# Kernel optimization log

Measured on AMD Instinct MI355X. Metric: run time of the kernel, lower is better.

The kernel has to match this reference:

```python
import jax, jax.numpy as jnp
import numpy as np

N, INSIZE, K, D = 512, 512, 64, 16


def setup_inputs() -> dict:
    key = jax.random.key(0)
    k1, k2, k3 = jax.random.split(key, 3)
    x = jax.random.normal(k1, (N, INSIZE), dtype=jnp.float32)
    W = jax.random.normal(k2, (K * D, INSIZE), dtype=jnp.float32) * (1.0 / np.sqrt(INSIZE))
    b = jax.random.normal(k3, (K * D,), dtype=jnp.float32) * 0.01
    return {"x": x, "W": W, "b": b}


def reference(x, W, b):
    # Linear: [N, insize] -> [N, K*D] -> [N, K, D]
    feat = (x @ W.T + b).reshape(-1, K, D)
    n = feat.shape[0]
    # Pairwise L1 distance over D: norm[i, k, j] = sum_d |feat[i,k,d] - feat[j,k,d]|
    # feature [N,K,D,1] vs feature_ [1,K,D,N] in the original broadcast
    diff = jnp.abs(feat[:, :, :, None] - jnp.transpose(feat, (1, 2, 0))[None])  # [N,K,D,N]
    norm = jnp.sum(diff, axis=2)  # [N,K,N]
    # Eraser: suppress self-similarity on the diagonal with a large penalty
    eraser = jnp.eye(n, dtype=feat.dtype)[:, None, :]  # [N,1,N]
    c_b = jnp.exp(-(norm + eraser * 1e6))
    o_b = jnp.sum(c_b, axis=2)  # [N,K]
    return jnp.concatenate((x, o_b), axis=1)  # [N, insize+K]
```

## Files before the change

kernel.cpp:

```cpp
#include <hip/hip_runtime.h>

#define NPTS 512
#define INS  512
#define KDIM 64
#define DDIM 16
#define CDIM (KDIM*DDIM)
#define OUTC (INS + KDIM)

__device__ __forceinline__ float exp2_fast(float x) {
    return __builtin_amdgcn_exp2f(x);
}

__global__ __launch_bounds__(256) void gemm_kernel(
    const float* __restrict__ x,
    const float* __restrict__ W,
    const float* __restrict__ bias,
    float* __restrict__ featT)
{
    const int tid = threadIdx.x;
    const int cbase = blockIdx.x * 64;
    const int ibase = blockIdx.y * 32;

    __shared__ float xs[16][32 + 2];
    __shared__ float wss[16][64 + 4];

    const int tx = tid & 15;
    const int ty = tid >> 4;

    float acc[2][4] = {};

    const int kkL = tid & 15;
    const int rL  = tid >> 4;

    for (int k0 = 0; k0 < INS; k0 += 16) {
        xs[kkL][rL]      = x[(ibase + rL) * INS + k0 + kkL];
        xs[kkL][rL + 16] = x[(ibase + rL + 16) * INS + k0 + kkL];
        wss[kkL][rL]      = W[(cbase + rL) * INS + k0 + kkL];
        wss[kkL][rL + 16] = W[(cbase + rL + 16) * INS + k0 + kkL];
        wss[kkL][rL + 32] = W[(cbase + rL + 32) * INS + k0 + kkL];
        wss[kkL][rL + 48] = W[(cbase + rL + 48) * INS + k0 + kkL];
        __syncthreads();

        #pragma unroll
        for (int kk = 0; kk < 16; ++kk) {
            float2 a = *(const float2*)&xs[kk][ty * 2];
            float4 w = *(const float4*)&wss[kk][tx * 4];
            acc[0][0] += a.x * w.x;  acc[0][1] += a.x * w.y;
            acc[0][2] += a.x * w.z;  acc[0][3] += a.x * w.w;
            acc[1][0] += a.y * w.x;  acc[1][1] += a.y * w.y;
            acc[1][2] += a.y * w.z;  acc[1][3] += a.y * w.w;
        }
        __syncthreads();
    }

    const float LOG2E = 1.4426950408889634f;
    const int c = cbase + tx * 4;
    float4 bq = *(const float4*)&bias[c];
    const int k = c >> 4;
    const int d = c & 15;
    #pragma unroll
    for (int ii = 0; ii < 2; ++ii) {
        const int i = ibase + ty * 2 + ii;
        float4 v;
        v.x = (acc[ii][0] + bq.x) * LOG2E;
        v.y = (acc[ii][1] + bq.y) * LOG2E;
        v.z = (acc[ii][2] + bq.z) * LOG2E;
        v.w = (acc[ii][3] + bq.w) * LOG2E;
        *(float4*)&featT[(k * NPTS + i) * DDIM + d] = v;
    }
}

__global__ __launch_bounds__(256) void pairwise_kernel(
    const float* __restrict__ featT,
    float* __restrict__ out)
{
    const int k = blockIdx.x;
    const int ibase = blockIdx.y * 64;

    __shared__ float fj[NPTS * DDIM];
    __shared__ float part[4][64];

    {
        const float4* src = (const float4*)(featT + (size_t)k * NPTS * DDIM);
        float4* dst = (float4*)fj;
        #pragma unroll
        for (int t = 0; t < 8; ++t)
            dst[threadIdx.x + t * 256] = src[threadIdx.x + t * 256];
    }

    const int lane = threadIdx.x & 63;
    const int wv   = threadIdx.x >> 6;
    const int i    = ibase + lane;

    float fi[16];
    {
        const float4* p = (const float4*)(featT + ((size_t)k * NPTS + i) * DDIM);
        float4 v0 = p[0], v1 = p[1], v2 = p[2], v3 = p[3];
        fi[0]=v0.x; fi[1]=v0.y; fi[2]=v0.z; fi[3]=v0.w;
        fi[4]=v1.x; fi[5]=v1.y; fi[6]=v1.z; fi[7]=v1.w;
        fi[8]=v2.x; fi[9]=v2.y; fi[10]=v2.z; fi[11]=v2.w;
        fi[12]=v3.x; fi[13]=v3.y; fi[14]=v3.z; fi[15]=v3.w;
    }
    __syncthreads();

    float acc0 = 0.f, acc1 = 0.f;
    const float* fp = fj + wv * 128 * DDIM;
    #pragma unroll 1
    for (int jj = 0; jj < 128; jj += 2) {
        {
            float n0=0.f, n1=0.f, n2=0.f, n3=0.f;
            #pragma unroll
            for (int d = 0; d < 4; ++d) {
                n0 += fabsf(fi[d]      - fp[d]);
                n1 += fabsf(fi[d + 4]  - fp[d + 4]);
                n2 += fabsf(fi[d + 8]  - fp[d + 8]);
                n3 += fabsf(fi[d + 12] - fp[d + 12]);
            }
            acc0 += exp2_fast(-((n0 + n1) + (n2 + n3)));
        }
        {
            float n0=0.f, n1=0.f, n2=0.f, n3=0.f;
            #pragma unroll
            for (int d = 0; d < 4; ++d) {
                n0 += fabsf(fi[d]      - fp[DDIM + d]);
                n1 += fabsf(fi[d + 4]  - fp[DDIM + d + 4]);
                n2 += fabsf(fi[d + 8]  - fp[DDIM + d + 8]);
                n3 += fabsf(fi[d + 12] - fp[DDIM + d + 12]);
            }
            acc1 += exp2_fast(-((n0 + n1) + (n2 + n3)));
        }
        fp += 2 * DDIM;
    }

    part[wv][lane] = acc0 + acc1;
    __syncthreads();

    if (wv == 0) {
        float o = ((part[0][lane] + part[1][lane]) + (part[2][lane] + part[3][lane])) - 1.0f;
        out[(size_t)i * OUTC + INS + k] = o;
    }
}

__global__ __launch_bounds__(256) void copy_x_kernel(
    const float* __restrict__ x, float* __restrict__ out)
{
    const int idx = blockIdx.x * 256 + threadIdx.x;
    const int i  = idx >> 7;
    const int j4 = idx & 127;
    ((float4*)out)[i * (OUTC / 4) + j4] = ((const float4*)x)[idx];
}

extern "C" void kernel_launch(void* const* d_in, const int* in_sizes, int n_in,
                              void* d_out, int out_size, void* d_ws, size_t ws_size,
                              hipStream_t stream) {
    const float* x    = (const float*)d_in[0];
    const float* W    = (const float*)d_in[1];
    const float* bias = (const float*)d_in[2];
    float* out = (float*)d_out;
    float* featT = (float*)d_ws;

    gemm_kernel<<<dim3(CDIM / 64, NPTS / 32), 256, 0, stream>>>(x, W, bias, featT);
    copy_x_kernel<<<dim3(NPTS * (INS / 4) / 256), 256, 0, stream>>>(x, out);
    pairwise_kernel<<<dim3(KDIM, NPTS / 64), 256, 0, stream>>>(featT, out);
}
```

Baseline: 106.2 us.

## Split-K GEMM into partial buffers and tile pairwise over j with atomics

The GEMM is split four ways along the input dimension. Each split writes a partial feature buffer, and the pairwise kernel sums the four partials when it loads them. The pairwise kernel is retiled so each block covers 128 i-rows against a 128-point j-quarter, with each thread handling two i rows per shared j load, and results are accumulated with atomicAdd into an output pre-initialized to -1. This raises the number of blocks and the register reuse of shared loads, at the cost of four times the workspace traffic, repeated partial summation in every block, and float atomics with nondeterministic ordering.

```diff
diff --git a/kernel.cpp b/kernel.cpp
--- a/kernel.cpp
+++ b/kernel.cpp
@@ -6,6 +6,8 @@
 #define DDIM 16
 #define CDIM (KDIM*DDIM)
 #define OUTC (INS + KDIM)
+#define KSPLIT 4
+#define FEAT_ELEMS ((size_t)NPTS * CDIM)
 
 __device__ __forceinline__ float exp2_fast(float x) {
     return __builtin_amdgcn_exp2f(x);
@@ -20,6 +22,7 @@
     const int tid = threadIdx.x;
     const int cbase = blockIdx.x * 64;
     const int ibase = blockIdx.y * 32;
+    const int kbase = blockIdx.z * (INS / KSPLIT);
 
     __shared__ float xs[16][32 + 2];
     __shared__ float wss[16][64 + 4];
@@ -32,7 +35,7 @@
     const int kkL = tid & 15;
     const int rL  = tid >> 4;
 
-    for (int k0 = 0; k0 < INS; k0 += 16) {
+    for (int k0 = kbase; k0 < kbase + INS / KSPLIT; k0 += 16) {
         xs[kkL][rL]      = x[(ibase + rL) * INS + k0 + kkL];
         xs[kkL][rL + 16] = x[(ibase + rL + 16) * INS + k0 + kkL];
         wss[kkL][rL]      = W[(cbase + rL) * INS + k0 + kkL];
@@ -54,100 +57,141 @@
     }
 
     const float LOG2E = 1.4426950408889634f;
+    const float bsel = (blockIdx.z == 0) ? 1.0f : 0.0f;
     const int c = cbase + tx * 4;
     float4 bq = *(const float4*)&bias[c];
     const int k = c >> 4;
     const int d = c & 15;
+    float* dst = featT + (size_t)blockIdx.z * FEAT_ELEMS;
     #pragma unroll
     for (int ii = 0; ii < 2; ++ii) {
         const int i = ibase + ty * 2 + ii;
         float4 v;
-        v.x = (acc[ii][0] + bq.x) * LOG2E;
-        v.y = (acc[ii][1] + bq.y) * LOG2E;
-        v.z = (acc[ii][2] + bq.z) * LOG2E;
-        v.w = (acc[ii][3] + bq.w) * LOG2E;
-        *(float4*)&featT[(k * NPTS + i) * DDIM + d] = v;
-    }
-}
-
-__global__ __launch_bounds__(256) void pairwise_kernel(
-    const float* __restrict__ featT,
+        v.x = (acc[ii][0] + bq.x * bsel) * LOG2E;
+        v.y = (acc[ii][1] + bq.y * bsel) * LOG2E;
+        v.z = (acc[ii][2] + bq.z * bsel) * LOG2E;
+        v.w = (acc[ii][3] + bq.w * bsel) * LOG2E;
+        *(float4*)&dst[((size_t)k * NPTS + i) * DDIM + d] = v;
+    }
+}
+
+__global__ __launch_bounds__(256) void init_out_kernel(
+    const float* __restrict__ x, float* __restrict__ out)
+{
+    const int idx = blockIdx.x * 256 + threadIdx.x;
+    const int i  = idx / (OUTC / 4);
+    const int j4 = idx - i * (OUTC / 4);
+    float4 v;
+    if (j4 < INS / 4) {
+        v = ((const float4*)x)[i * (INS / 4) + j4];
+    } else {
+        v = make_float4(-1.0f, -1.0f, -1.0f, -1.0f);
+    }
+    ((float4*)out)[idx] = v;
+}
+
+__device__ __forceinline__ void load_feat16(
+    const float* f0, const float* f1, const float* f2, const float* f3,
+    size_t off, float* fi)
+{
+    #pragma unroll
+    for (int q = 0; q < 4; ++q) {
+        float4 a = *(const float4*)(f0 + off + q * 4);
+        float4 b = *(const float4*)(f1 + off + q * 4);
+        float4 c = *(const float4*)(f2 + off + q * 4);
+        float4 d = *(const float4*)(f3 + off + q * 4);
+        fi[q * 4 + 0] = (a.x + b.x) + (c.x + d.x);
+        fi[q * 4 + 1] = (a.y + b.y) + (c.y + d.y);
+        fi[q * 4 + 2] = (a.z + b.z) + (c.z + d.z);
+        fi[q * 4 + 3] = (a.w + b.w) + (c.w + d.w);
+    }
+}
+
+__global__ __launch_bounds__(256, 4) void pairwise_kernel(
+    const float* __restrict__ f0, const float* __restrict__ f1,
+    const float* __restrict__ f2, const float* __restrict__ f3,
     float* __restrict__ out)
 {
-    const int k = blockIdx.x;
-    const int ibase = blockIdx.y * 64;
-
-    __shared__ float fj[NPTS * DDIM];
-    __shared__ float part[4][64];
+    const int k     = blockIdx.x;
+    const int itile = blockIdx.y;
+    const int jq    = blockIdx.z;
+
+    __shared__ float fj[128 * DDIM];
+    __shared__ float part[4][128];
 
     {
-        const float4* src = (const float4*)(featT + (size_t)k * NPTS * DDIM);
+        const size_t base = ((size_t)k * NPTS + jq * 128) * DDIM;
+        const float4* s0 = (const float4*)(f0 + base);
+        const float4* s1 = (const float4*)(f1 + base);
+        const float4* s2 = (const float4*)(f2 + base);
+        const float4* s3 = (const float4*)(f3 + base);
         float4* dst = (float4*)fj;
         #pragma unroll
-        for (int t = 0; t < 8; ++t)
-            dst[threadIdx.x + t * 256] = src[threadIdx.x + t * 256];
+        for (int u = 0; u < 2; ++u) {
+            int idx = threadIdx.x + u * 256;
+            float4 a = s0[idx], b = s1[idx], c = s2[idx], d = s3[idx];
+            float4 r;
+            r.x = (a.x + b.x) + (c.x + d.x);
+            r.y = (a.y + b.y) + (c.y + d.y);
+            r.z = (a.z + b.z) + (c.z + d.z);
+            r.w = (a.w + b.w) + (c.w + d.w);
+            dst[idx] = r;
+        }
     }
 
     const int lane = threadIdx.x & 63;
     const int wv   = threadIdx.x >> 6;
-    const int i    = ibase + lane;
-
-    float fi[16];
-    {
-        const float4* p = (const float4*)(featT + ((size_t)k * NPTS + i) * DDIM);
-        float4 v0 = p[0], v1 = p[1], v2 = p[2], v3 = p[3];
-        fi[0]=v0.x; fi[1]=v0.y; fi[2]=v0.z; fi[3]=v0.w;
-        fi[4]=v1.x; fi[5]=v1.y; fi[6]=v1.z; fi[7]=v1.w;
-        fi[8]=v2.x; fi[9]=v2.y; fi[10]=v2.z; fi[11]=v2.w;
-        fi[12]=v3.x; fi[13]=v3.y; fi[14]=v3.z; fi[15]=v3.w;
-    }
+    const int i0   = itile * 128 + lane;
+    const int i1   = i0 + 64;
+
+    float fi0[16], fi1[16];
+    load_feat16(f0, f1, f2, f3, ((size_t)k * NPTS + i0) * DDIM, fi0);
+    load_feat16(f0, f1, f2, f3, ((size_t)k * NPTS + i1) * DDIM, fi1);
     __syncthreads();
 
     float acc0 = 0.f, acc1 = 0.f;
-    const float* fp = fj + wv * 128 * DDIM;
-    #pragma unroll 1
-    for (int jj = 0; jj < 128; jj += 2) {
+    const float* fp = fj + wv * 32 * DDIM;
+    #pragma unroll 2
+    for (int jj = 0; jj < 32; ++jj) {
+        const float* p = fp + jj * DDIM;
+        float4 q0 = *(const float4*)(p);
+        float4 q1 = *(const float4*)(p + 4);
+        float4 q2 = *(const float4*)(p + 8);
+        float4 q3 = *(const float4*)(p + 12);
         {
-            float n0=0.f, n1=0.f, n2=0.f, n3=0.f;
-            #pragma unroll
-            for (int d = 0; d < 4; ++d) {
-                n0 += fabsf(fi[d]      - fp[d]);
-                n1 += fabsf(fi[d + 4]  - fp[d + 4]);
-                n2 += fabsf(fi[d + 8]  - fp[d + 8]);
-                n3 += fabsf(fi[d + 12] - fp[d + 12]);
-            }
-            acc0 += exp2_fast(-((n0 + n1) + (n2 + n3)));
+            float a0 = fabsf(fi0[0]  - q0.x) + fabsf(fi0[1]  - q0.y)
+                     + fabsf(fi0[2]  - q0.z) + fabsf(fi0[3]  - q0.w);
+            float a1 = fabsf(fi0[4]  - q1.x) + fabsf(fi0[5]  - q1.y)
+                     + fabsf(fi0[6]  - q1.z) + fabsf(fi0[7]  - q1.w);
+            float a2 = fabsf(fi0[8]  - q2.x) + fabsf(fi0[9]  - q2.y)
+                     + fabsf(fi0[10] - q2.z) + fabsf(fi0[11] - q2.w);
+            float a3 = fabsf(fi0[12] - q3.x) + fabsf(fi0[13] - q3.y)
+                     + fabsf(fi0[14] - q3.z) + fabsf(fi0[15] - q3.w);
+            acc0 += exp2_fast(-((a0 + a1) + (a2 + a3)));
         }
         {
-            float n0=0.f, n1=0.f, n2=0.f, n3=0.f;
-            #pragma unroll
-            for (int d = 0; d < 4; ++d) {
-                n0 += fabsf(fi[d]      - fp[DDIM + d]);
-                n1 += fabsf(fi[d + 4]  - fp[DDIM + d + 4]);
-                n2 += fabsf(fi[d + 8]  - fp[DDIM + d + 8]);
-                n3 += fabsf(fi[d + 12] - fp[DDIM + d + 12]);
-            }
-            acc1 += exp2_fast(-((n0 + n1) + (n2 + n3)));
-        }
-        fp += 2 * DDIM;
-    }
-
-    part[wv][lane] = acc0 + acc1;
+            float b0 = fabsf(fi1[0]  - q0.x) + fabsf(fi1[1]  - q0.y)
+                     + fabsf(fi1[2]  - q0.z) + fabsf(fi1[3]  - q0.w);
+            float b1 = fabsf(fi1[4]  - q1.x) + fabsf(fi1[5]  - q1.y)
+                     + fabsf(fi1[6]  - q1.z) + fabsf(fi1[7]  - q1.w);
+            float b2 = fabsf(fi1[8]  - q2.x) + fabsf(fi1[9]  - q2.y)
+                     + fabsf(fi1[10] - q2.z) + fabsf(fi1[11] - q2.w);
+            float b3 = fabsf(fi1[12] - q3.x) + fabsf(fi1[13] - q3.y)
+                     + fabsf(fi1[14] - q3.z) + fabsf(fi1[15] - q3.w);
+            acc1 += exp2_fast(-((b0 + b1) + (b2 + b3)));
+        }
+    }
+
+    part[wv][lane]      = acc0;
+    part[wv][lane + 64] = acc1;
     __syncthreads();
 
-    if (wv == 0) {
-        float o = ((part[0][lane] + part[1][lane]) + (part[2][lane] + part[3][lane])) - 1.0f;
-        out[(size_t)i * OUTC + INS + k] = o;
-    }
-}
-
-__global__ __launch_bounds__(256) void copy_x_kernel(
-    const float* __restrict__ x, float* __restrict__ out)
-{
-    const int idx = blockIdx.x * 256 + threadIdx.x;
-    const int i  = idx >> 7;
-    const int j4 = idx & 127;
-    ((float4*)out)[i * (OUTC / 4) + j4] = ((const float4*)x)[idx];
+    if (threadIdx.x < 128) {
+        float s = (part[0][threadIdx.x] + part[1][threadIdx.x])
+                + (part[2][threadIdx.x] + part[3][threadIdx.x]);
+        const int i = itile * 128 + threadIdx.x;
+        atomicAdd(&out[(size_t)i * OUTC + INS + k], s);
+    }
 }
 
 extern "C" void kernel_launch(void* const* d_in, const int* in_sizes, int n_in,
@@ -159,7 +203,8 @@
     float* out = (float*)d_out;
     float* featT = (float*)d_ws;
 
-    gemm_kernel<<<dim3(CDIM / 64, NPTS / 32), 256, 0, stream>>>(x, W, bias, featT);
-    copy_x_kernel<<<dim3(NPTS * (INS / 4) / 256), 256, 0, stream>>>(x, out);
-    pairwise_kernel<<<dim3(KDIM, NPTS / 64), 256, 0, stream>>>(featT, out);
-}
+    gemm_kernel<<<dim3(CDIM / 64, NPTS / 32, KSPLIT), 256, 0, stream>>>(x, W, bias, featT);
+    init_out_kernel<<<dim3(NPTS * (OUTC / 4) / 256), 256, 0, stream>>>(x, out);
+    pairwise_kernel<<<dim3(KDIM, 4, 4), 256, 0, stream>>>(
+        featT, featT + FEAT_ELEMS, featT + 2 * FEAT_ELEMS, featT + 3 * FEAT_ELEMS, out);
+}
```

Result: faster. 97.68 us (-8.0%).

## Split-K GEMM, fused reduce/init kernel, and j-split pairwise with atomics

Applied to the files above, without the earlier changes.

The GEMM becomes split-K with 8 partial outputs and larger 64x64 tiles. A new kernel reduces the partials, adds bias and the log2e scale, copies x into the output, and initialises the o_b columns to -1. The pairwise kernel now splits j into 8 chunks, and each thread handles 4 i rows to reuse j loads from shared memory. Partial sums are accumulated into the output with atomicAdd. This raises parallelism and cuts shared-memory footprint, at the cost of extra workspace traffic, atomics, and nondeterministic summation order.

```diff
diff --git a/kernel.cpp b/kernel.cpp
--- a/kernel.cpp
+++ b/kernel.cpp
@@ -6,148 +6,174 @@
 #define DDIM 16
 #define CDIM (KDIM*DDIM)
 #define OUTC (INS + KDIM)
+#define KSPLIT 8
+#define FEAT_ELEMS ((size_t)NPTS * CDIM)
+#define FEAT_F4    (FEAT_ELEMS / 4)
 
 __device__ __forceinline__ float exp2_fast(float x) {
     return __builtin_amdgcn_exp2f(x);
 }
 
+__device__ __forceinline__ void fma2(float2& acc, float s, float x, float y) {
+    acc.x = __builtin_fmaf(s, x, acc.x);
+    acc.y = __builtin_fmaf(s, y, acc.y);
+}
+
 __global__ __launch_bounds__(256) void gemm_kernel(
     const float* __restrict__ x,
     const float* __restrict__ W,
-    const float* __restrict__ bias,
     float* __restrict__ featT)
 {
     const int tid = threadIdx.x;
     const int cbase = blockIdx.x * 64;
-    const int ibase = blockIdx.y * 32;
+    const int ibase = blockIdx.y * 64;
+    const int kbase = blockIdx.z * (INS / KSPLIT);
 
-    __shared__ float xs[16][32 + 2];
-    __shared__ float wss[16][64 + 4];
+    __shared__ float xs[16][68];
+    __shared__ float wss[16][68];
 
     const int tx = tid & 15;
     const int ty = tid >> 4;
-
-    float acc[2][4] = {};
-
     const int kkL = tid & 15;
     const int rL  = tid >> 4;
 
-    for (int k0 = 0; k0 < INS; k0 += 16) {
-        xs[kkL][rL]      = x[(ibase + rL) * INS + k0 + kkL];
-        xs[kkL][rL + 16] = x[(ibase + rL + 16) * INS + k0 + kkL];
-        wss[kkL][rL]      = W[(cbase + rL) * INS + k0 + kkL];
-        wss[kkL][rL + 16] = W[(cbase + rL + 16) * INS + k0 + kkL];
-        wss[kkL][rL + 32] = W[(cbase + rL + 32) * INS + k0 + kkL];
-        wss[kkL][rL + 48] = W[(cbase + rL + 48) * INS + k0 + kkL];
+    float2 acc[4][2] = {};
+
+    for (int k0 = kbase; k0 < kbase + INS / KSPLIT; k0 += 16) {
+        #pragma unroll
+        for (int q = 0; q < 4; ++q) {
+            xs[kkL][rL + 16 * q]  = x[(ibase + rL + 16 * q) * INS + k0 + kkL];
+            wss[kkL][rL + 16 * q] = W[(cbase + rL + 16 * q) * INS + k0 + kkL];
+        }
         __syncthreads();
 
         #pragma unroll
         for (int kk = 0; kk < 16; ++kk) {
-            float2 a = *(const float2*)&xs[kk][ty * 2];
+            float4 a = *(const float4*)&xs[kk][ty * 4];
             float4 w = *(const float4*)&wss[kk][tx * 4];
-            acc[0][0] += a.x * w.x;  acc[0][1] += a.x * w.y;
-            acc[0][2] += a.x * w.z;  acc[0][3] += a.x * w.w;
-            acc[1][0] += a.y * w.x;  acc[1][1] += a.y * w.y;
-            acc[1][2] += a.y * w.z;  acc[1][3] += a.y * w.w;
+            fma2(acc[0][0], a.x, w.x, w.y);  fma2(acc[0][1], a.x, w.z, w.w);
+            fma2(acc[1][0], a.y, w.x, w.y);  fma2(acc[1][1], a.y, w.z, w.w);
+            fma2(acc[2][0], a.z, w.x, w.y);  fma2(acc[2][1], a.z, w.z, w.w);
+            fma2(acc[3][0], a.w, w.x, w.y);  fma2(acc[3][1], a.w, w.z, w.w);
         }
         __syncthreads();
     }
 
-    const float LOG2E = 1.4426950408889634f;
     const int c = cbase + tx * 4;
-    float4 bq = *(const float4*)&bias[c];
     const int k = c >> 4;
     const int d = c & 15;
+    float* dst = featT + (size_t)blockIdx.z * FEAT_ELEMS;
     #pragma unroll
-    for (int ii = 0; ii < 2; ++ii) {
-        const int i = ibase + ty * 2 + ii;
-        float4 v;
-        v.x = (acc[ii][0] + bq.x) * LOG2E;
-        v.y = (acc[ii][1] + bq.y) * LOG2E;
-        v.z = (acc[ii][2] + bq.z) * LOG2E;
-        v.w = (acc[ii][3] + bq.w) * LOG2E;
-        *(float4*)&featT[(k * NPTS + i) * DDIM + d] = v;
+    for (int ii = 0; ii < 4; ++ii) {
+        const int i = ibase + ty * 4 + ii;
+        float4 v = make_float4(acc[ii][0].x, acc[ii][0].y, acc[ii][1].x, acc[ii][1].y);
+        *(float4*)&dst[((size_t)k * NPTS + i) * DDIM + d] = v;
     }
 }
 
-__global__ __launch_bounds__(256) void pairwise_kernel(
+__global__ __launch_bounds__(256) void fuse_reduce_init_kernel(
     const float* __restrict__ featT,
+    const float* __restrict__ bias,
+    const float* __restrict__ x,
+    float* __restrict__ featR,
     float* __restrict__ out)
 {
-    const int k = blockIdx.x;
-    const int ibase = blockIdx.y * 64;
+    const int b = blockIdx.x;
+    if (b < 512) {
+        const int f4 = b * 256 + threadIdx.x;
+        const float4* s = (const float4*)featT;
+        float4 p0 = s[f4];
+        float4 p1 = s[f4 + 1 * FEAT_F4];
+        float4 p2 = s[f4 + 2 * FEAT_F4];
+        float4 p3 = s[f4 + 3 * FEAT_F4];
+        float4 p4 = s[f4 + 4 * FEAT_F4];
+        float4 p5 = s[f4 + 5 * FEAT_F4];
+        float4 p6 = s[f4 + 6 * FEAT_F4];
+        float4 p7 = s[f4 + 7 * FEAT_F4];
+        const int k = f4 >> 11;
+        const float4 bq = ((const float4*)bias)[(k << 2) + (f4 & 3)];
+        const float LOG2E = 1.4426950408889634f;
+        float4 r;
+        r.x = (((p0.x + p1.x) + (p2.x + p3.x)) + ((p4.x + p5.x) + (p6.x + p7.x)) + bq.x) * LOG2E;
+        r.y = (((p0.y + p1.y) + (p2.y + p3.y)) + ((p4.y + p5.y) + (p6.y + p7.y)) + bq.y) * LOG2E;
+        r.z = (((p0.z + p1.z) + (p2.z + p3.z)) + ((p4.z + p5.z) + (p6.z + p7.z)) + bq.z) * LOG2E;
+        r.w = (((p0.w + p1.w) + (p2.w + p3.w)) + ((p4.w + p5.w) + (p6.w + p7.w)) + bq.w) * LOG2E;
+        ((float4*)featR)[f4] = r;
+    } else {
+        const int idx = (b - 512) * 256 + threadIdx.x;
+        const int i  = idx / (OUTC / 4);
+        const int j4 = idx - i * (OUTC / 4);
+        float4 v;
+        if (j4 < INS / 4) v = ((const float4*)x)[i * (INS / 4) + j4];
+        else              v = make_float4(-1.0f, -1.0f, -1.0f, -1.0f);
+        ((float4*)out)[idx] = v;
+    }
+}
 
-    __shared__ float fj[NPTS * DDIM];
-    __shared__ float part[4][64];
+__global__ __launch_bounds__(256, 4) void pairwise_kernel(
+    const float* __restrict__ featR,
+    float* __restrict__ out)
+{
+    const int k     = blockIdx.x;
+    const int itile = blockIdx.y;
+    const int jq    = blockIdx.z;
 
-    {
-        const float4* src = (const float4*)(featT + (size_t)k * NPTS * DDIM);
-        float4* dst = (float4*)fj;
-        #pragma unroll
-        for (int t = 0; t < 8; ++t)
-            dst[threadIdx.x + t * 256] = src[threadIdx.x + t * 256];
-    }
+    __shared__ float fj[64 * DDIM];
+    __shared__ float part[4][256];
+
+    ((float4*)fj)[threadIdx.x] =
+        ((const float4*)(featR + ((size_t)k * NPTS + jq * 64) * DDIM))[threadIdx.x];
 
     const int lane = threadIdx.x & 63;
     const int wv   = threadIdx.x >> 6;
-    const int i    = ibase + lane;
 
-    float fi[16];
-    {
-        const float4* p = (const float4*)(featT + ((size_t)k * NPTS + i) * DDIM);
+    float fi[4][16];
+    #pragma unroll
+    for (int u = 0; u < 4; ++u) {
+        const int i = itile * 256 + u * 64 + lane;
+        const float4* p = (const float4*)(featR + ((size_t)k * NPTS + i) * DDIM);
         float4 v0 = p[0], v1 = p[1], v2 = p[2], v3 = p[3];
-        fi[0]=v0.x; fi[1]=v0.y; fi[2]=v0.z; fi[3]=v0.w;
-        fi[4]=v1.x; fi[5]=v1.y; fi[6]=v1.z; fi[7]=v1.w;
-        fi[8]=v2.x; fi[9]=v2.y; fi[10]=v2.z; fi[11]=v2.w;
-        fi[12]=v3.x; fi[13]=v3.y; fi[14]=v3.z; fi[15]=v3.w;
+        fi[u][0]=v0.x;  fi[u][1]=v0.y;  fi[u][2]=v0.z;  fi[u][3]=v0.w;
+        fi[u][4]=v1.x;  fi[u][5]=v1.y;  fi[u][6]=v1.z;  fi[u][7]=v1.w;
+        fi[u][8]=v2.x;  fi[u][9]=v2.y;  fi[u][10]=v2.z; fi[u][11]=v2.w;
+        fi[u][12]=v3.x; fi[u][13]=v3.y; fi[u][14]=v3.z; fi[u][15]=v3.w;
     }
     __syncthreads();
 
-    float acc0 = 0.f, acc1 = 0.f;
-    const float* fp = fj + wv * 128 * DDIM;
-    #pragma unroll 1
-    for (int jj = 0; jj < 128; jj += 2) {
-        {
-            float n0=0.f, n1=0.f, n2=0.f, n3=0.f;
-            #pragma unroll
-            for (int d = 0; d < 4; ++d) {
-                n0 += fabsf(fi[d]      - fp[d]);
-                n1 += fabsf(fi[d + 4]  - fp[d + 4]);
-                n2 += fabsf(fi[d + 8]  - fp[d + 8]);
-                n3 += fabsf(fi[d + 12] - fp[d + 12]);
-            }
-            acc0 += exp2_fast(-((n0 + n1) + (n2 + n3)));
+    float acc[4] = {0.f, 0.f, 0.f, 0.f};
+    const float* fp = fj + wv * 16 * DDIM;
+    #pragma unroll 2
+    for (int jj = 0; jj < 16; ++jj) {
+        const float* p = fp + jj * DDIM;
+        float4 q0 = *(const float4*)(p);
+        float4 q1 = *(const float4*)(p + 4);
+        float4 q2 = *(const float4*)(p + 8);
+        float4 q3 = *(const float4*)(p + 12);
+        #pragma unroll
+        for (int u = 0; u < 4; ++u) {
+            float a0 = fabsf(fi[u][0]  - q0.x) + fabsf(fi[u][1]  - q0.y)
+                     + fabsf(fi[u][2]  - q0.z) + fabsf(fi[u][3]  - q0.w);
+            float a1 = fabsf(fi[u][4]  - q1.x) + fabsf(fi[u][5]  - q1.y)
+                     + fabsf(fi[u][6]  - q1.z) + fabsf(fi[u][7]  - q1.w);
+            float a2 = fabsf(fi[u][8]  - q2.x) + fabsf(fi[u][9]  - q2.y)
+                     + fabsf(fi[u][10] - q2.z) + fabsf(fi[u][11] - q2.w);
+            float a3 = fabsf(fi[u][12] - q3.x) + fabsf(fi[u][13] - q3.y)
+                     + fabsf(fi[u][14] - q3.z) + fabsf(fi[u][15] - q3.w);
+            acc[u] += exp2_fast(-((a0 + a1) + (a2 + a3)));
         }
-        {
-            float n0=0.f, n1=0.f, n2=0.f, n3=0.f;
-            #pragma unroll
-            for (int d = 0; d < 4; ++d) {
-                n0 += fabsf(fi[d]      - fp[DDIM + d]);
-                n1 += fabsf(fi[d + 4]  - fp[DDIM + d + 4]);
-                n2 += fabsf(fi[d + 8]  - fp[DDIM + d + 8]);
-                n3 += fabsf(fi[d + 12] - fp[DDIM + d + 12]);
-            }
-            acc1 += exp2_fast(-((n0 + n1) + (n2 + n3)));
-        }
-        fp += 2 * DDIM;
     }
 
-    part[wv][lane] = acc0 + acc1;
+    #pragma unroll
+    for (int u = 0; u < 4; ++u)
+        part[wv][u * 64 + lane] = acc[u];
     __syncthreads();
 
-    if (wv == 0) {
-        float o = ((part[0][lane] + part[1][lane]) + (part[2][lane] + part[3][lane])) - 1.0f;
-        out[(size_t)i * OUTC + INS + k] = o;
+    {
+        const int t = threadIdx.x;
+        float s = (part[0][t] + part[1][t]) + (part[2][t] + part[3][t]);
+        const int i = itile * 256 + t;
+        atomicAdd(&out[(size_t)i * OUTC + INS + k], s);
     }
-}
-
-__global__ __launch_bounds__(256) void copy_x_kernel(
-    const float* __restrict__ x, float* __restrict__ out)
-{
-    const int idx = blockIdx.x * 256 + threadIdx.x;
-    const int i  = idx >> 7;
-    const int j4 = idx & 127;
-    ((float4*)out)[i * (OUTC / 4) + j4] = ((const float4*)x)[idx];
 }
 
 extern "C" void kernel_launch(void* const* d_in, const int* in_sizes, int n_in,
@@ -158,8 +184,10 @@
     const float* bias = (const float*)d_in[2];
     float* out = (float*)d_out;
     float* featT = (float*)d_ws;
+    float* featR = featT + KSPLIT * FEAT_ELEMS;
 
-    gemm_kernel<<<dim3(CDIM / 64, NPTS / 32), 256, 0, stream>>>(x, W, bias, featT);
-    copy_x_kernel<<<dim3(NPTS * (INS / 4) / 256), 256, 0, stream>>>(x, out);
-    pairwise_kernel<<<dim3(KDIM, NPTS / 64), 256, 0, stream>>>(featT, out);
+    gemm_kernel<<<dim3(CDIM / 64, NPTS / 64, KSPLIT), 256, 0, stream>>>(x, W, featT);
+    fuse_reduce_init_kernel<<<dim3(512 + NPTS * (OUTC / 4) / 256), 256, 0, stream>>>(
+        featT, bias, x, featR, out);
+    pairwise_kernel<<<dim3(KDIM, 2, 8), 256, 0, stream>>>(featR, out);
 }
```

Measured after the change: 109.0 us. 2.6% more time.
